# Performance work log

Hardware: AMD Instinct MI355X
Metric: run time of the kernel (lower is better)

The kernel has to match this reference:

```python
import jax, jax.numpy as jnp
import numpy as np

D = 1024      # input_size / d_model
H = 16        # num_heads
HD = D // H   # head_size = 64
T = 2048      # block_size / seq_len
B = 2
FF = 4 * D
EPS = 1e-5


def setup_inputs() -> dict:
    key = jax.random.key(0)
    ks = jax.random.split(key, 16)
    s_in = 1.0 / np.sqrt(D)
    s_ff = 1.0 / np.sqrt(FF)
    return {
        "x": jax.random.normal(ks[0], (B, T, D), dtype=jnp.float32),
        # per-head unbiased projections, stacked over heads: [H, D, HD]
        "wq": jax.random.normal(ks[1], (H, D, HD), dtype=jnp.float32) * s_in,
        "wk": jax.random.normal(ks[2], (H, D, HD), dtype=jnp.float32) * s_in,
        "wv": jax.random.normal(ks[3], (H, D, HD), dtype=jnp.float32) * s_in,
        "w_proj": jax.random.normal(ks[4], (D, D), dtype=jnp.float32) * s_in,
        "b_proj": jnp.zeros((D,), dtype=jnp.float32),
        "ln1_g": jnp.ones((D,), dtype=jnp.float32),
        "ln1_b": jnp.zeros((D,), dtype=jnp.float32),
        "ln2_g": jnp.ones((D,), dtype=jnp.float32),
        "ln2_b": jnp.zeros((D,), dtype=jnp.float32),
        "w1": jax.random.normal(ks[5], (D, FF), dtype=jnp.float32) * s_in,
        "b1": jnp.zeros((FF,), dtype=jnp.float32),
        "w2": jax.random.normal(ks[6], (FF, D), dtype=jnp.float32) * s_ff,
        "b2": jnp.zeros((D,), dtype=jnp.float32),
    }


def _layernorm(x, g, b):
    mu = jnp.mean(x, axis=-1, keepdims=True)
    var = jnp.mean(jnp.square(x - mu), axis=-1, keepdims=True)
    return (x - mu) * jax.lax.rsqrt(var + EPS) * g + b


def reference(x, wq, wk, wv, w_proj, b_proj, ln1_g, ln1_b, ln2_g, ln2_b, w1, b1, w2, b2):
    Bv, Tv, _ = x.shape
    h = _layernorm(x, ln1_g, ln1_b)                       # [B,T,D]
    q = jnp.einsum("btc,hcd->bhtd", h, wq)
    k = jnp.einsum("btc,hcd->bhtd", h, wk)
    v = jnp.einsum("btc,hcd->bhtd", h, wv)
    scores = jnp.einsum("bhtd,bhsd->bhts", q, k) * (HD ** -0.5)  # [B,H,T,T]
    causal = jnp.tril(jnp.ones((Tv, Tv), dtype=bool))
    scores = jnp.where(causal, scores, -jnp.inf)
    attn = jax.nn.softmax(scores, axis=-1)
    out = jnp.einsum("bhts,bhsd->bhtd", attn, v)          # [B,H,T,HD]
    out = out.transpose(0, 2, 1, 3).reshape(Bv, Tv, H * HD)  # concat heads
    out = out @ w_proj + b_proj
    x = x + out
    h2 = _layernorm(x, ln2_g, ln2_b)
    ff = jax.nn.gelu(h2 @ w1 + b1, approximate=False) @ w2 + b2
    return x + ff
```

## Files before the change

### kernel.cpp

```cpp
#include <hip/hip_runtime.h>
#include <hip/hip_bf16.h>
#include <cstdint>
#include <cstddef>
#include <math.h>

#define D_ 1024
#define H_ 16
#define HD_ 64
#define T_ 2048
#define B_ 2
#define FF_ 4096
#define BT_ (B_*T_)
#define NT_ 32

typedef unsigned short u16;
typedef __attribute__((ext_vector_type(8))) __bf16 bf16x8;
typedef __attribute__((ext_vector_type(8))) u16 u16x8;
typedef __attribute__((ext_vector_type(4))) float f32x4;

__device__ __forceinline__ u16 f2bf(float f) {
  unsigned u = __builtin_bit_cast(unsigned, f);
  u += 0x7FFFu + ((u >> 16) & 1u);
  return (u16)(u >> 16);
}

__device__ __forceinline__ unsigned cvt_pk_bf16(float a, float b) {
  unsigned r;
  asm("v_cvt_pk_bf16_f32 %0, %1, %2" : "=v"(r) : "v"(a), "v"(b));
  return r;
}

__device__ __forceinline__ void gload16(const void* g, void* l) {
  __builtin_amdgcn_global_load_lds((__attribute__((address_space(1))) void*)g,
                                   (__attribute__((address_space(3))) void*)l, 16, 0, 0);
}

__global__ __launch_bounds__(256) void transpose_all(
    const float* __restrict__ wq, const float* __restrict__ wk,
    const float* __restrict__ wv, const float* __restrict__ w_proj,
    const float* __restrict__ w1, const float* __restrict__ w2,
    u16* __restrict__ wqkv_t, u16* __restrict__ wproj_t,
    u16* __restrict__ w1t, u16* __restrict__ w2t) {
  __shared__ float tile[32][33];
  const int bid = blockIdx.x;
  const float* in; u16* out; int R, C, tx, ty;
  if (bid < 3072) {
    const int w = bid >> 10, rem = bid & 1023;
    const int z = rem >> 6, t = rem & 63;
    tx = t & 1; ty = t >> 1;
    R = D_; C = HD_;
    in  = (w == 0 ? wq : w == 1 ? wk : wv) + (size_t)z * R * C;
    out = wqkv_t + (size_t)w * D_ * D_ + (size_t)z * C * R;
  } else if (bid < 4096) {
    const int t = bid - 3072;
    tx = t & 31; ty = t >> 5;
    R = D_; C = D_; in = w_proj; out = wproj_t;
  } else if (bid < 8192) {
    const int t = bid - 4096;
    tx = t & 127; ty = t >> 7;
    R = D_; C = FF_; in = w1; out = w1t;
  } else {
    const int t = bid - 8192;
    tx = t & 31; ty = t >> 5;
    R = FF_; C = D_; in = w2; out = w2t;
  }
  const int x = tx * 32 + threadIdx.x;
  const int y0 = ty * 32 + threadIdx.y;
  #pragma unroll
  for (int j = 0; j < 32; j += 8)
    tile[threadIdx.y + j][threadIdx.x] = in[(size_t)(y0 + j) * C + x];
  __syncthreads();
  const int orr = ty * 32 + threadIdx.x;
  const int oc0 = tx * 32 + threadIdx.y;
  #pragma unroll
  for (int j = 0; j < 32; j += 8)
    out[(size_t)(oc0 + j) * R + orr] = f2bf(tile[threadIdx.x][threadIdx.y + j]);
}

__global__ __launch_bounds__(256) void ln_rows(const float* __restrict__ x,
    const float* __restrict__ g, const float* __restrict__ bb, u16* __restrict__ out) {
  const int row = blockIdx.x, tid = threadIdx.x;
  const float4 v = ((const float4*)(x + (size_t)row * D_))[tid];
  float s = v.x + v.y + v.z + v.w;
  float sq = v.x*v.x + v.y*v.y + v.z*v.z + v.w*v.w;
  #pragma unroll
  for (int m = 1; m < 64; m <<= 1) { s += __shfl_xor(s, m); sq += __shfl_xor(sq, m); }
  __shared__ float ss[4], qs[4];
  if ((tid & 63) == 0) { ss[tid >> 6] = s; qs[tid >> 6] = sq; }
  __syncthreads();
  s  = ss[0] + ss[1] + ss[2] + ss[3];
  sq = qs[0] + qs[1] + qs[2] + qs[3];
  const float mean = s * (1.f / D_);
  const float var  = sq * (1.f / D_) - mean * mean;
  const float rstd = rsqrtf(var + 1e-5f);
  const float4 gv = ((const float4*)g)[tid];
  const float4 bv = ((const float4*)bb)[tid];
  u16 o[4];
  o[0] = f2bf((v.x - mean) * rstd * gv.x + bv.x);
  o[1] = f2bf((v.y - mean) * rstd * gv.y + bv.y);
  o[2] = f2bf((v.z - mean) * rstd * gv.z + bv.z);
  o[3] = f2bf((v.w - mean) * rstd * gv.w + bv.w);
  *(ushort4*)(out + (size_t)row * D_ + tid * 4) = *(ushort4*)o;
}

template<int ACT, int BIAS, int OUTBF, int PARTIAL>
__global__ __launch_bounds__(256, 2) void gemm128(
    const u16* __restrict__ A, const u16* __restrict__ Bt,
    const float* __restrict__ bias, const float* resid,
    void* Cout, int M, int N, int K, int Kper) {
  __shared__ __attribute__((aligned(16))) u16 LA[2][128 * 64];
  __shared__ __attribute__((aligned(16))) u16 LB[2][128 * 64];

  const int tid = threadIdx.x;
  const int wid = tid >> 6, lane = tid & 63;
  const int wr = wid >> 1, wc = wid & 1;
  const int frow = lane & 15, hi = lane >> 4;

  const int gx = gridDim.x;
  const int nwg = gx * gridDim.y;
  const int orig = blockIdx.y * gx + blockIdx.x;
  const int cpx = nwg >> 3;
  const int swz = (orig & 7) * cpx + (orig >> 3);
  const int bm = (swz / gx) * 128, bn = (swz % gx) * 128;
  const int z = PARTIAL ? blockIdx.z : 0;
  const int koff = z * Kper;
  const int nt = Kper >> 6;

  const u16* Atile = A + (size_t)bm * K + koff;
  const u16* Btile = Bt + (size_t)bn * K + koff;

  const int srow = tid >> 3;
  const int gch  = (tid & 7) ^ (srow & 7);

  f32x4 acc[4][4] = {};

  #define STAGE128(kt, db)                                                        \
    {                                                                             \
      _Pragma("unroll")                                                           \
      for (int j = 0; j < 4; j++) {                                               \
        const int rw = j * 32;                                                    \
        gload16(Atile + (size_t)(rw + srow) * K + (size_t)(kt) * 64 + gch * 8,    \
                &LA[db][(rw + wid * 8) * 64]);                                    \
        gload16(Btile + (size_t)(rw + srow) * K + (size_t)(kt) * 64 + gch * 8,    \
                &LB[db][(rw + wid * 8) * 64]);                                    \
      }                                                                           \
    }

  STAGE128(0, 0);
  asm volatile("s_waitcnt vmcnt(0)" ::: "memory");
  __builtin_amdgcn_s_barrier();

  for (int t = 0; t < nt; ++t) {
    const int db = t & 1;
    if (t + 1 < nt) {
      STAGE128(t + 1, db ^ 1);
      asm volatile("s_waitcnt vmcnt(8)" ::: "memory");
    } else {
      asm volatile("s_waitcnt vmcnt(0)" ::: "memory");
    }
    __builtin_amdgcn_s_barrier();

    const u16* Ab = &LA[db][0];
    const u16* Bb = &LB[db][0];

    bf16x8 bfr[4][2];
    #pragma unroll
    for (int ni = 0; ni < 4; ni++)
      #pragma unroll
      for (int ks = 0; ks < 2; ks++) {
        const int row = wc * 64 + ni * 16 + frow;
        bfr[ni][ks] = *(const bf16x8*)(Bb + row * 64 + (((ks * 4 + hi) ^ (row & 7)) << 3));
      }
    #pragma unroll
    for (int half = 0; half < 2; half++) {
      bf16x8 af[2][2];
      #pragma unroll
      for (int m2 = 0; m2 < 2; m2++)
        #pragma unroll
        for (int ks = 0; ks < 2; ks++) {
          const int row = wr * 64 + (half * 2 + m2) * 16 + frow;
          af[m2][ks] = *(const bf16x8*)(Ab + row * 64 + (((ks * 4 + hi) ^ (row & 7)) << 3));
        }
      __builtin_amdgcn_s_setprio(1);
      #pragma unroll
      for (int m2 = 0; m2 < 2; m2++)
        #pragma unroll
        for (int ni = 0; ni < 4; ni++)
          #pragma unroll
          for (int ks = 0; ks < 2; ks++)
            acc[half * 2 + m2][ni] =
                __builtin_amdgcn_mfma_f32_16x16x32_bf16(af[m2][ks], bfr[ni][ks],
                                                        acc[half * 2 + m2][ni], 0, 0, 0);
      __builtin_amdgcn_s_setprio(0);
    }
    __builtin_amdgcn_s_barrier();
  }
  #undef STAGE128

  const int r0 = bm + wr * 64 + hi * 4;
  const int c0 = bn + wc * 64 + frow;
  #pragma unroll
  for (int mi = 0; mi < 4; mi++) {
    #pragma unroll
    for (int ni = 0; ni < 4; ni++) {
      #pragma unroll
      for (int r = 0; r < 4; r++) {
        float v = acc[mi][ni][r];
        const int rr = r0 + mi * 16 + r;
        const int cc = c0 + ni * 16;
        if (PARTIAL) {
          ((float*)Cout)[((size_t)z * M + rr) * N + cc] = v;
        } else {
          if (BIAS) v += bias[cc];
          if (ACT == 1) {
            const float u = v * (0.79788456f + 0.03567740814f * v * v);
            const float e = exp2f(fminf(u * 2.885390082f, 80.f));
            v = v * e / (e + 1.0f);
          }
          if (resid) v += resid[(size_t)rr * N + cc];
          if (OUTBF) ((u16*)Cout)[(size_t)rr * N + cc] = f2bf(v);
          else       ((float*)Cout)[(size_t)rr * N + cc] = v;
        }
      }
    }
  }
}

template<int NPART>
__global__ __launch_bounds__(256) void reduce_parts(
    const float* __restrict__ parts, const float* __restrict__ bias,
    const float* __restrict__ resid, float* __restrict__ out, int MN, int N) {
  const int i4 = (blockIdx.x * 256 + threadIdx.x) * 4;
  if (i4 >= MN) return;
  float4 s = *(const float4*)(parts + i4);
  #pragma unroll
  for (int p = 1; p < NPART; p++) {
    const float4 t = *(const float4*)(parts + (size_t)p * MN + i4);
    s.x += t.x; s.y += t.y; s.z += t.z; s.w += t.w;
  }
  const float4 bv = *(const float4*)(bias + (i4 & (N - 1)));
  const float4 rv = *(const float4*)(resid + i4);
  s.x += bv.x + rv.x; s.y += bv.y + rv.y; s.z += bv.z + rv.z; s.w += bv.w + rv.w;
  *(float4*)(out + i4) = s;
}

__global__ __launch_bounds__(256) void reduce2_ln(
    const float* __restrict__ parts, const float* __restrict__ bias,
    const float* __restrict__ resid, const float* __restrict__ g,
    const float* __restrict__ bb, float* __restrict__ xout,
    u16* __restrict__ h2, int MN) {
  const int row = blockIdx.x, tid = threadIdx.x;
  const int i4 = row * D_ + tid * 4;
  float4 s = *(const float4*)(parts + i4);
  const float4 t = *(const float4*)(parts + (size_t)MN + i4);
  const float4 bv = *(const float4*)(bias + tid * 4);
  const float4 rv = *(const float4*)(resid + i4);
  s.x += t.x + bv.x + rv.x; s.y += t.y + bv.y + rv.y;
  s.z += t.z + bv.z + rv.z; s.w += t.w + bv.w + rv.w;
  *(float4*)(xout + i4) = s;
  float sm = s.x + s.y + s.z + s.w;
  float sq = s.x*s.x + s.y*s.y + s.z*s.z + s.w*s.w;
  #pragma unroll
  for (int m = 1; m < 64; m <<= 1) { sm += __shfl_xor(sm, m); sq += __shfl_xor(sq, m); }
  __shared__ float ss[4], qs[4];
  if ((tid & 63) == 0) { ss[tid >> 6] = sm; qs[tid >> 6] = sq; }
  __syncthreads();
  sm = ss[0] + ss[1] + ss[2] + ss[3];
  sq = qs[0] + qs[1] + qs[2] + qs[3];
  const float mean = sm * (1.f / D_);
  const float var  = sq * (1.f / D_) - mean * mean;
  const float rstd = rsqrtf(var + 1e-5f);
  const float4 gv = ((const float4*)g)[tid];
  const float4 b2v = ((const float4*)bb)[tid];
  u16 o[4];
  o[0] = f2bf((s.x - mean) * rstd * gv.x + b2v.x);
  o[1] = f2bf((s.y - mean) * rstd * gv.y + b2v.y);
  o[2] = f2bf((s.z - mean) * rstd * gv.z + b2v.z);
  o[3] = f2bf((s.w - mean) * rstd * gv.w + b2v.w);
  *(ushort4*)(h2 + (size_t)row * D_ + tid * 4) = *(ushort4*)o;
}

__global__ __launch_bounds__(256) void repack_qkv(const u16* __restrict__ qkv,
    u16* __restrict__ q, u16* __restrict__ k, u16* __restrict__ vt) {
  const int t0 = blockIdx.x * 64, bh = blockIdx.y;
  const int b = bh >> 4, h = bh & 15;
  const int tid = threadIdx.x;
  const int c = (tid & 7) * 8;
  __shared__ __attribute__((aligned(16))) u16 vs[64][72];
  #pragma unroll
  for (int p = 0; p < 2; p++) {
    const int tl = p * 32 + (tid >> 3);
    const size_t inrow = ((size_t)b * T_ + t0 + tl) * 3072 + h * 64;
    u16x8 qv = *(const u16x8*)(qkv + inrow + c);
    bf16x8 kv = *(const bf16x8*)(qkv + inrow + 1024 + c);
    bf16x8 vv = *(const bf16x8*)(qkv + inrow + 2048 + c);
    alignas(16) u16 qs[8];
    #pragma unroll
    for (int e = 0; e < 8; e++) {
      const float f = __builtin_bit_cast(float, ((unsigned)qv[e]) << 16) * 0.18033688011112042f;
      qs[e] = f2bf(f);
    }
    *(u16x8*)(q + ((size_t)bh * T_ + t0 + tl) * HD_ + c) = *(u16x8*)qs;
    *(bf16x8*)(k + ((size_t)bh * T_ + t0 + tl) * HD_ + c) = kv;
    *(bf16x8*)&vs[tl][c] = vv;
  }
  __syncthreads();
  const int d = tid >> 2, tc = (tid & 3) * 16;
  alignas(16) u16 tmp[16];
  #pragma unroll
  for (int j = 0; j < 16; j++) tmp[j] = vs[tc + j][d];
  *(bf16x8*)(vt + ((size_t)bh * HD_ + d) * T_ + t0 + tc)     = *(bf16x8*)&tmp[0];
  *(bf16x8*)(vt + ((size_t)bh * HD_ + d) * T_ + t0 + tc + 8) = *(bf16x8*)&tmp[8];
}

__global__ __launch_bounds__(512) void attn_fwd(
    const u16* __restrict__ q, const u16* __restrict__ k,
    const u16* __restrict__ vt, u16* __restrict__ out) {
  __shared__ __attribute__((aligned(16))) u16 Ps[8][16 * 64];
  __shared__ __attribute__((aligned(16))) u16 Kb[2][64 * 64];
  __shared__ __attribute__((aligned(16))) u16 Vb[2][64 * 64];

  const int bid = blockIdx.x;
  const int xcd = bid & 7, j = bid >> 3;
  const int bh  = xcd + 8 * (j & 3);
  const int qb  = 15 - (j >> 2);
  const int b = bh >> 4, h = bh & 15;
  const int tid = threadIdx.x, wid = tid >> 6, lane = tid & 63;
  const u16* kh = k  + (size_t)bh * T_ * HD_;
  const u16* vh = vt + (size_t)bh * HD_ * T_;
  const int q0 = qb * 128;
  const int nkt = 2 * qb + 2;
  const int wlast = 2 * qb + (wid >> 2);

  const int frow = lane & 15;
  const int hi   = lane >> 4;
  const int fk   = hi * 8;
  const int rowb = hi * 4;
  const int colb = frow;
  const int srow = tid >> 3;
  const int gch  = (tid & 7) ^ (srow & 7);

  u16x8 onebits = (u16x8)((u16)0x3F80);
  bf16x8 b_one = (frow == 0) ? __builtin_bit_cast(bf16x8, onebits) : (bf16x8){};

  u16* Pw = &Ps[wid][0];

  const u16* qrow = q + ((size_t)bh * T_ + q0 + wid * 16 + frow) * HD_;
  bf16x8 aq[2];
  aq[0] = *(const bf16x8*)(qrow + fk);
  aq[1] = *(const bf16x8*)(qrow + 32 + fk);

  float m2[4] = {-3e38f, -3e38f, -3e38f, -3e38f};
  f32x4 acc_l = {};
  f32x4 acc_o[4] = {};

  int cur = 0;
  gload16(kh + (size_t)srow * HD_ + gch * 8, &Kb[0][(wid * 8) * 64]);
  gload16(vh + (size_t)srow * T_ + gch * 8,  &Vb[0][(wid * 8) * 64]);
  __syncthreads();

  for (int kt = 0; kt < nkt; ++kt) {
    if (kt + 1 < nkt) {
      const int nx = cur ^ 1, ktn = kt + 1;
      gload16(kh + (size_t)(ktn * 64 + srow) * HD_ + gch * 8, &Kb[nx][(wid * 8) * 64]);
      gload16(vh + (size_t)srow * T_ + ktn * 64 + gch * 8,    &Vb[nx][(wid * 8) * 64]);
    }

    if (kt <= wlast) {
      const u16* Kc = &Kb[cur][0];
      const u16* Vc = &Vb[cur][0];

      float p2[4][4];
      __builtin_amdgcn_s_setprio(1);
      #pragma unroll
      for (int ni = 0; ni < 4; ni++) {
        f32x4 s = {};
        #pragma unroll
        for (int ks = 0; ks < 2; ks++) {
          const int row = ni * 16 + frow;
          const int ch  = ks * 4 + hi;
          bf16x8 bk = *(const bf16x8*)(Kc + row * 64 + ((ch ^ (row & 7)) << 3));
          s = __builtin_amdgcn_mfma_f32_16x16x32_bf16(aq[ks], bk, s, 0, 0, 0);
        }
        #pragma unroll
        for (int r = 0; r < 4; r++) p2[ni][r] = s[r];
      }
      __builtin_amdgcn_s_setprio(0);

      if (kt >= nkt - 2) {
        #pragma unroll
        for (int ni = 0; ni < 4; ni++)
          #pragma unroll
          for (int r = 0; r < 4; r++) {
            const bool msk = (kt * 64 + ni * 16 + colb) > (q0 + wid * 16 + rowb + r);
            if (msk) p2[ni][r] = -3e38f;
          }
      }

      float lmax[4];
      #pragma unroll
      for (int r = 0; r < 4; r++)
        lmax[r] = fmaxf(fmaxf(p2[0][r], p2[1][r]), fmaxf(p2[2][r], p2[3][r]));
      int ok = 1;
      #pragma unroll
      for (int r = 0; r < 4; r++) ok &= (lmax[r] <= m2[r] + 8.0f);
      if (!__all(ok)) {
        #pragma unroll
        for (int r = 0; r < 4; r++) {
          float rm = lmax[r];
          rm = fmaxf(rm, __shfl_xor(rm, 1));
          rm = fmaxf(rm, __shfl_xor(rm, 2));
          rm = fmaxf(rm, __shfl_xor(rm, 4));
          rm = fmaxf(rm, __shfl_xor(rm, 8));
          const float mnew = fmaxf(m2[r], rm);
          const float corr = exp2f(m2[r] - mnew);
          m2[r] = mnew;
          acc_l[r] *= corr;
          #pragma unroll
          for (int ni = 0; ni < 4; ni++) acc_o[ni][r] *= corr;
        }
      }
      #pragma unroll
      for (int ni = 0; ni < 4; ni++)
        #pragma unroll
        for (int r = 0; r < 4; r++) p2[ni][r] = exp2f(p2[ni][r] - m2[r]);

      #pragma unroll
      for (int ni = 0; ni < 4; ni++) {
        #pragma unroll
        for (int r = 0; r < 4; r += 2) {
          const unsigned pk = cvt_pk_bf16(p2[ni][r], p2[ni][r + 1]);
          const int lr0 = rowb + r, lr1 = rowb + r + 1;
          const int ch = ni * 2 + (colb >> 3);
          Pw[lr0 * 64 + ((ch ^ (lr0 & 7)) << 3) + (colb & 7)] = (u16)pk;
          Pw[lr1 * 64 + ((ch ^ (lr1 & 7)) << 3) + (colb & 7)] = (u16)(pk >> 16);
        }
      }
      bf16x8 ap[2];
      {
        const int c0 = (0 * 4 + hi) ^ (frow & 7);
        const int c1 = (1 * 4 + hi) ^ (frow & 7);
        ap[0] = *(const bf16x8*)(Pw + frow * 64 + (c0 << 3));
        ap[1] = *(const bf16x8*)(Pw + frow * 64 + (c1 << 3));
      }

      __builtin_amdgcn_s_setprio(1);
      #pragma unroll
      for (int ks = 0; ks < 2; ks++)
        acc_l = __builtin_amdgcn_mfma_f32_16x16x32_bf16(ap[ks], b_one, acc_l, 0, 0, 0);
      #pragma unroll
      for (int ni = 0; ni < 4; ni++) {
        #pragma unroll
        for (int ks = 0; ks < 2; ks++) {
          const int row = ni * 16 + frow;
          const int ch  = ks * 4 + hi;
          bf16x8 bv = *(const bf16x8*)(Vc + row * 64 + ((ch ^ (row & 7)) << 3));
          acc_o[ni] = __builtin_amdgcn_mfma_f32_16x16x32_bf16(ap[ks], bv, acc_o[ni], 0, 0, 0);
        }
      }
      __builtin_amdgcn_s_setprio(0);
    }

    __syncthreads();
    cur ^= 1;
  }

  float linv[4];
  #pragma unroll
  for (int r = 0; r < 4; r++) {
    const float lv = __shfl(acc_l[r], lane & 48);
    linv[r] = 1.0f / lv;
  }
  #pragma unroll
  for (int ni = 0; ni < 4; ni++)
    #pragma unroll
    for (int r = 0; r < 4; r++) {
      const float ov = acc_o[ni][r] * linv[r];
      const size_t row = (size_t)b * T_ + q0 + wid * 16 + rowb + r;
      out[row * D_ + h * HD_ + ni * 16 + colb] = f2bf(ov);
    }
}

extern "C" void kernel_launch(void* const* d_in, const int* in_sizes, int n_in,
                              void* d_out, int out_size, void* d_ws, size_t ws_size,
                              hipStream_t stream) {
  (void)in_sizes; (void)n_in; (void)out_size; (void)ws_size;
  const float* x      = (const float*)d_in[0];
  const float* wq     = (const float*)d_in[1];
  const float* wk     = (const float*)d_in[2];
  const float* wv     = (const float*)d_in[3];
  const float* w_proj = (const float*)d_in[4];
  const float* b_proj = (const float*)d_in[5];
  const float* ln1_g  = (const float*)d_in[6];
  const float* ln1_b  = (const float*)d_in[7];
  const float* ln2_g  = (const float*)d_in[8];
  const float* ln2_b  = (const float*)d_in[9];
  const float* w1     = (const float*)d_in[10];
  const float* b1     = (const float*)d_in[11];
  const float* w2     = (const float*)d_in[12];
  const float* b2     = (const float*)d_in[13];

  uint8_t* ws = (uint8_t*)d_ws;
  const size_t MB = 1024 * 1024;
  u16* wqkv_t = (u16*)(ws + 0);
  u16* wproj_t = (u16*)(ws + 6 * MB);
  u16* w1t  = (u16*)(ws + 8 * MB);
  u16* w2t  = (u16*)(ws + 16 * MB);
  u16* hbuf = (u16*)(ws + 24 * MB);
  u16* qkv  = (u16*)(ws + 32 * MB);
  u16* qb   = (u16*)(ws + 56 * MB);
  u16* kb   = (u16*)(ws + 64 * MB);
  u16* vtb  = (u16*)(ws + 72 * MB);
  u16* aout = (u16*)(ws + 80 * MB);
  u16* h2   = (u16*)(ws + 88 * MB);
  u16* ff1  = (u16*)(ws + 96 * MB);
  float* pparts = (float*)(ws + 32 * MB);
  float* fparts = (float*)(ws + 32 * MB);
  float* xout = (float*)d_out;

  transpose_all<<<12288, dim3(32, 8), 0, stream>>>(
      wq, wk, wv, w_proj, w1, w2, wqkv_t, wproj_t, w1t, w2t);

  ln_rows<<<BT_, 256, 0, stream>>>(x, ln1_g, ln1_b, hbuf);

  gemm128<0,0,1,0><<<dim3(3072/128, BT_/128), 256, 0, stream>>>(
      hbuf, wqkv_t, nullptr, nullptr, qkv, BT_, 3072, D_, D_);

  repack_qkv<<<dim3(T_/64, B_*H_), 256, 0, stream>>>(qkv, qb, kb, vtb);

  attn_fwd<<<dim3(512), 512, 0, stream>>>(qb, kb, vtb, aout);

  gemm128<0,0,0,1><<<dim3(D_/128, BT_/128, 2), 256, 0, stream>>>(
      aout, wproj_t, nullptr, nullptr, pparts, BT_, D_, D_, D_/2);
  reduce2_ln<<<BT_, 256, 0, stream>>>(
      pparts, b_proj, x, ln2_g, ln2_b, xout, h2, BT_*D_);

  gemm128<1,1,1,0><<<dim3(FF_/128, BT_/128), 256, 0, stream>>>(
      h2, w1t, b1, nullptr, ff1, BT_, FF_, D_, D_);

  gemm128<0,0,0,1><<<dim3(D_/128, BT_/128, 4), 256, 0, stream>>>(
      ff1, w2t, nullptr, nullptr, fparts, BT_, D_, FF_, FF_/4);
  reduce_parts<4><<<(BT_*D_)/1024, 256, 0, stream>>>(
      fparts, b2, xout, xout, BT_*D_, D_);
}
```

Before: 259.3 us.

## Halve GEMM K-tile to 32 and raise occupancy to four blocks per CU

```diff
diff --git a/kernel.cpp b/kernel.cpp
--- a/kernel.cpp
+++ b/kernel.cpp
@@ -104,12 +104,12 @@
 }
 
 template<int ACT, int BIAS, int OUTBF, int PARTIAL>
-__global__ __launch_bounds__(256, 2) void gemm128(
+__global__ __launch_bounds__(256, 4) void gemm128(
     const u16* __restrict__ A, const u16* __restrict__ Bt,
     const float* __restrict__ bias, const float* resid,
     void* Cout, int M, int N, int K, int Kper) {
-  __shared__ __attribute__((aligned(16))) u16 LA[2][128 * 64];
-  __shared__ __attribute__((aligned(16))) u16 LB[2][128 * 64];
+  __shared__ __attribute__((aligned(16))) u16 LA[2][128 * 32];
+  __shared__ __attribute__((aligned(16))) u16 LB[2][128 * 32];
 
   const int tid = threadIdx.x;
   const int wid = tid >> 6, lane = tid & 63;
@@ -124,37 +124,34 @@
   const int bm = (swz / gx) * 128, bn = (swz % gx) * 128;
   const int z = PARTIAL ? blockIdx.z : 0;
   const int koff = z * Kper;
-  const int nt = Kper >> 6;
-
-  const u16* Atile = A + (size_t)bm * K + koff;
-  const u16* Btile = Bt + (size_t)bn * K + koff;
-
-  const int srow = tid >> 3;
-  const int gch  = (tid & 7) ^ (srow & 7);
+  const int nt = Kper >> 5;
+
+  const int srow = tid >> 2;
+  const int gch  = (tid & 3) ^ (srow & 3);
+  const u16* Ag0 = A + (size_t)(bm + srow) * K + koff + gch * 8;
+  const u16* Ag1 = Ag0 + (size_t)64 * K;
+  const u16* Bg0 = Bt + (size_t)(bn + srow) * K + koff + gch * 8;
+  const u16* Bg1 = Bg0 + (size_t)64 * K;
+  const int ldsA0 = (wid * 16) * 32, ldsA1 = (64 + wid * 16) * 32;
 
   f32x4 acc[4][4] = {};
 
-  #define STAGE128(kt, db)                                                        \
-    {                                                                             \
-      _Pragma("unroll")                                                           \
-      for (int j = 0; j < 4; j++) {                                               \
-        const int rw = j * 32;                                                    \
-        gload16(Atile + (size_t)(rw + srow) * K + (size_t)(kt) * 64 + gch * 8,    \
-                &LA[db][(rw + wid * 8) * 64]);                                    \
-        gload16(Btile + (size_t)(rw + srow) * K + (size_t)(kt) * 64 + gch * 8,    \
-                &LB[db][(rw + wid * 8) * 64]);                                    \
-      }                                                                           \
-    }
-
-  STAGE128(0, 0);
-  asm volatile("s_waitcnt vmcnt(0)" ::: "memory");
-  __builtin_amdgcn_s_barrier();
+  #define STAGE32(kt, db)                              \
+    {                                                  \
+      const int ko = (kt) * 32;                        \
+      gload16(Ag0 + ko, &LA[db][ldsA0]);               \
+      gload16(Ag1 + ko, &LA[db][ldsA1]);               \
+      gload16(Bg0 + ko, &LB[db][ldsA0]);               \
+      gload16(Bg1 + ko, &LB[db][ldsA1]);               \
+    }
+
+  STAGE32(0, 0);
 
   for (int t = 0; t < nt; ++t) {
     const int db = t & 1;
     if (t + 1 < nt) {
-      STAGE128(t + 1, db ^ 1);
-      asm volatile("s_waitcnt vmcnt(8)" ::: "memory");
+      STAGE32(t + 1, db ^ 1);
+      asm volatile("s_waitcnt vmcnt(4)" ::: "memory");
     } else {
       asm volatile("s_waitcnt vmcnt(0)" ::: "memory");
     }
@@ -163,39 +160,24 @@
     const u16* Ab = &LA[db][0];
     const u16* Bb = &LB[db][0];
 
-    bf16x8 bfr[4][2];
+    bf16x8 af[4], bfr[4];
     #pragma unroll
-    for (int ni = 0; ni < 4; ni++)
-      #pragma unroll
-      for (int ks = 0; ks < 2; ks++) {
-        const int row = wc * 64 + ni * 16 + frow;
-        bfr[ni][ks] = *(const bf16x8*)(Bb + row * 64 + (((ks * 4 + hi) ^ (row & 7)) << 3));
-      }
+    for (int i = 0; i < 4; i++) {
+      const int ra = wr * 64 + i * 16 + frow;
+      af[i]  = *(const bf16x8*)(Ab + ra * 32 + ((hi ^ (ra & 3)) << 3));
+      const int rb = wc * 64 + i * 16 + frow;
+      bfr[i] = *(const bf16x8*)(Bb + rb * 32 + ((hi ^ (rb & 3)) << 3));
+    }
+    __builtin_amdgcn_s_setprio(1);
     #pragma unroll
-    for (int half = 0; half < 2; half++) {
-      bf16x8 af[2][2];
-      #pragma unroll
-      for (int m2 = 0; m2 < 2; m2++)
-        #pragma unroll
-        for (int ks = 0; ks < 2; ks++) {
-          const int row = wr * 64 + (half * 2 + m2) * 16 + frow;
-          af[m2][ks] = *(const bf16x8*)(Ab + row * 64 + (((ks * 4 + hi) ^ (row & 7)) << 3));
-        }
-      __builtin_amdgcn_s_setprio(1);
-      #pragma unroll
-      for (int m2 = 0; m2 < 2; m2++)
-        #pragma unroll
-        for (int ni = 0; ni < 4; ni++)
-          #pragma unroll
-          for (int ks = 0; ks < 2; ks++)
-            acc[half * 2 + m2][ni] =
-                __builtin_amdgcn_mfma_f32_16x16x32_bf16(af[m2][ks], bfr[ni][ks],
-                                                        acc[half * 2 + m2][ni], 0, 0, 0);
-      __builtin_amdgcn_s_setprio(0);
-    }
+    for (int mi = 0; mi < 4; mi++)
+      #pragma unroll
+      for (int ni = 0; ni < 4; ni++)
+        acc[mi][ni] = __builtin_amdgcn_mfma_f32_16x16x32_bf16(af[mi], bfr[ni], acc[mi][ni], 0, 0, 0);
+    __builtin_amdgcn_s_setprio(0);
     __builtin_amdgcn_s_barrier();
   }
-  #undef STAGE128
+  #undef STAGE32
 
   const int r0 = bm + wr * 64 + hi * 4;
   const int c0 = bn + wc * 64 + frow;
@@ -215,7 +197,7 @@
           if (ACT == 1) {
             const float u = v * (0.79788456f + 0.03567740814f * v * v);
             const float e = exp2f(fminf(u * 2.885390082f, 80.f));
-            v = v * e / (e + 1.0f);
+            v = v - v * __builtin_amdgcn_rcpf(1.0f + e);
           }
           if (resid) v += resid[(size_t)rr * N + cc];
           if (OUTBF) ((u16*)Cout)[(size_t)rr * N + cc] = f2bf(v);
```

New measurement: 249.2 us. 1.04x faster.
